# Optimization experiments

Measured on AMD Instinct MI355X. Metric: run time of the kernel, lower is better.

## Reference

```python
import jax, jax.numpy as jnp
import numpy as np

DIM = 1024
NUM_HEADS = 16
HEAD_DIM = DIM // NUM_HEADS


def setup_inputs() -> dict:
    key = jax.random.key(0)
    ks = jax.random.split(key, 5)
    scale = 1.0 / np.sqrt(DIM)
    return {
        "x": jax.random.normal(ks[0], (2, 2048, DIM), dtype=jnp.float32),
        "qkv_w": jax.random.normal(ks[1], (3 * DIM, DIM), dtype=jnp.float32) * scale,
        "qkv_b": jax.random.normal(ks[2], (3 * DIM,), dtype=jnp.float32) * 0.01,
        "proj_w": jax.random.normal(ks[3], (DIM, DIM), dtype=jnp.float32) * scale,
        "proj_b": jax.random.normal(ks[4], (DIM,), dtype=jnp.float32) * 0.01,
    }


def reference(x, qkv_w, qkv_b, proj_w, proj_b):
    B, N, D = x.shape
    H, Hd = NUM_HEADS, HEAD_DIM
    # fused QKV projection: [B,N,3D]
    qkv = jnp.einsum('bnd,ed->bne', x, qkv_w) + qkv_b
    qkv = qkv.reshape(B, N, 3, H, Hd)
    q = qkv[:, :, 0].transpose(0, 2, 1, 3)  # [B,H,N,Hd]
    k = qkv[:, :, 1].transpose(0, 2, 1, 3)
    v = qkv[:, :, 2].transpose(0, 2, 1, 3)
    scale = 1.0 / jnp.sqrt(jnp.asarray(Hd, dtype=x.dtype))
    scores = jnp.einsum('bhqd,bhkd->bhqk', q, k) * scale  # [B,H,N,N]
    attn = jax.nn.softmax(scores, axis=-1)
    out = jnp.einsum('bhqk,bhkd->bhqd', attn, v)  # [B,H,N,Hd]
    out = out.transpose(0, 2, 1, 3).reshape(B, N, D)
    return jnp.einsum('bnd,ed->bne', out, proj_w) + proj_b
```

## Files before the change

kernel.cpp:

```cpp
#include <hip/hip_runtime.h>
#include <hip/hip_bf16.h>
#include <stdint.h>


typedef __bf16 bf16;
typedef __bf16 bf16x2 __attribute__((ext_vector_type(2)));
typedef __bf16 bf16x4 __attribute__((ext_vector_type(4)));
typedef __bf16 bf16x8 __attribute__((ext_vector_type(8)));
typedef float  f32x4  __attribute__((ext_vector_type(4)));
typedef float  f32x16 __attribute__((ext_vector_type(16)));
typedef uint32_t u32x4 __attribute__((ext_vector_type(4)));

#define QSCALE 0.18033688011112042f

__device__ __forceinline__ void gload_lds16(const void* g, void* l) {
    __builtin_amdgcn_global_load_lds(
        (const __attribute__((address_space(1))) void*)(uintptr_t)g,
        (__attribute__((address_space(3))) void*)(uint32_t)(uintptr_t)l,
        16, 0, 0);
}

__device__ __forceinline__ uint32_t pkbf(float a, float b) {
    bf16x2 t = { (bf16)a, (bf16)b };
    return __builtin_bit_cast(uint32_t, t);
}

__global__ void cast_all(const float* __restrict__ x,
                         const float* __restrict__ qw,
                         const float* __restrict__ pw,
                         bf16* __restrict__ xb, bf16* __restrict__ wq,
                         bf16* __restrict__ wp) {
    int i = blockIdx.x * blockDim.x + threadIdx.x;
    const float4* src; bf16x4* dst; int off;
    if (i < 1048576)      { src = (const float4*)x;  dst = (bf16x4*)xb; off = i; }
    else if (i < 1835008) { src = (const float4*)qw; dst = (bf16x4*)wq; off = i - 1048576; }
    else                  { src = (const float4*)pw; dst = (bf16x4*)wp; off = i - 1835008; }
    float4 v = src[off];
    bf16x4 o = { (bf16)v.x, (bf16)v.y, (bf16)v.z, (bf16)v.w };
    dst[off] = o;
}

template<int EPI>
__global__ __launch_bounds__(256) void gemm128(
    const bf16* __restrict__ A,
    const bf16* __restrict__ Bw,
    const float* __restrict__ bias,
    float* __restrict__ outF,
    bf16* __restrict__ qb, bf16* __restrict__ kf, bf16* __restrict__ vf,
    int K)
{
    __shared__ __align__(16) char gsm[EPI == 0 ? 36864 : 32768];
    bf16* ct = (bf16*)gsm;
    const int tid  = threadIdx.x;
    const int lane = tid & 63, w = tid >> 6;
    const int g = lane >> 4, lr = lane & 15;
    const int wr = w >> 1, wc = w & 1;
    int mt, nt;
    if (EPI == 0) {
        int bid = blockIdx.x;
        int xcd = bid & 7, i = bid >> 3;
        mt = xcd * 4 + i / 24;
        nt = i % 24;
    } else {
        nt = blockIdx.x; mt = blockIdx.y;
    }
    const int mbase = mt * 128, nbase = nt * 128;

    f32x4 acc[4][4] = {};

    auto stg = [&](int buf, int it) {
        const bf16* Ag = A  + (size_t)mbase * K + it * 32;
        const bf16* Bg = Bw + (size_t)nbase * K + it * 32;
        bf16* as = (bf16*)(gsm + buf * 16384);
        bf16* bs = (bf16*)(gsm + buf * 16384 + 8192);
        int c0 = tid, c1 = 256 + tid;
        gload_lds16(Ag + (size_t)(c0 >> 2) * K + (c0 & 3) * 8, as + c0 * 8);
        gload_lds16(Bg + (size_t)(c0 >> 2) * K + (c0 & 3) * 8, bs + c0 * 8);
        gload_lds16(Ag + (size_t)(c1 >> 2) * K + (c1 & 3) * 8, as + c1 * 8);
        gload_lds16(Bg + (size_t)(c1 >> 2) * K + (c1 & 3) * 8, bs + c1 * 8);
    };

    const int nIt = K >> 5;
    stg(0, 0);
    __syncthreads();

    #pragma unroll 2
    for (int it = 0; it < nIt; ++it) {
        const int cur = it & 1;
        if (it + 1 < nIt) stg(cur ^ 1, it + 1);

        const bf16* as = (const bf16*)(gsm + cur * 16384);
        const bf16* bs = as + 4096;
        bf16x8 af[4], bfr[4];
        #pragma unroll
        for (int mi = 0; mi < 4; ++mi)
            af[mi] = *(const bf16x8*)(as + (wr * 64 + mi * 16 + lr) * 32 + g * 8);
        #pragma unroll
        for (int ni = 0; ni < 4; ++ni)
            bfr[ni] = *(const bf16x8*)(bs + (wc * 64 + ni * 16 + lr) * 32 + g * 8);
        #pragma unroll
        for (int mi = 0; mi < 4; ++mi)
            #pragma unroll
            for (int ni = 0; ni < 4; ++ni)
                acc[mi][ni] = __builtin_amdgcn_mfma_f32_16x16x32_bf16(
                    af[mi], bfr[ni], acc[mi][ni], 0, 0, 0);

        __syncthreads();
    }

    if (EPI == 1) {
        #pragma unroll
        for (int ni = 0; ni < 4; ++ni) {
            int e = nbase + wc * 64 + ni * 16 + lr;
            float bv = bias[e];
            #pragma unroll
            for (int mi = 0; mi < 4; ++mi) {
                #pragma unroll
                for (int r = 0; r < 4; ++r) {
                    int token = mbase + wr * 64 + mi * 16 + g * 4 + r;
                    outF[(size_t)token * 1024 + e] = acc[mi][ni][r] + bv;
                }
            }
        }
    } else {
        const int sec = nbase >> 10;
        #pragma unroll
        for (int ni = 0; ni < 4; ++ni) {
            int ec = wc * 64 + ni * 16 + lr;
            float bv = bias[nbase + ec];
            #pragma unroll
            for (int mi = 0; mi < 4; ++mi) {
                #pragma unroll
                for (int r = 0; r < 4; ++r) {
                    int tl = wr * 64 + mi * 16 + g * 4 + r;
                    float v = acc[mi][ni][r] + bv;
                    if (sec == 0) v *= QSCALE;
                    int row = (sec == 2) ? ec : tl;
                    int col = (sec == 2) ? tl : ec;
                    ct[row * 144 + col] = (bf16)v;
                }
            }
        }
        __syncthreads();
        const int b  = mbase >> 11;
        const int h0 = (nbase & 1023) >> 6;
        const int mb = mbase & 2047;
        #pragma unroll
        for (int si = 0; si < 8; ++si) {
            int c   = si * 256 + tid;
            int hh  = c >> 10;
            int w10 = c & 1023;
            int bh  = b * 16 + h0 + hh;
            int lrow, lcol;
            size_t gaddr;
            bf16* dst;
            if (sec == 0) {
                int nl = w10 >> 3, d0 = (w10 & 7) * 8;
                lrow = nl; lcol = hh * 64 + d0;
                gaddr = ((size_t)bh * 2048 + mb + nl) * 64 + d0;
                dst = qb;
            } else if (sec == 1) {
                int o = w10 * 8;
                int frag = o >> 9, l = (o >> 3) & 63;
                int nl = (frag >> 2) * 32 + (l & 31);
                int d0 = (frag & 3) * 16 + (l >> 5) * 8;
                lrow = nl; lcol = hh * 64 + d0;
                gaddr = ((size_t)(bh * 64 + (mb >> 5))) * 2048 + o;
                dst = kf;
            } else {
                int o = w10 * 8;
                int n6 = o >> 12, r2 = o & 4095;
                int d5 = r2 >> 11, r3 = r2 & 2047;
                int nc = r3 >> 9,  l  = (r3 >> 3) & 63;
                int d  = d5 * 32 + (l & 31);
                int n0 = n6 * 64 + nc * 16 + (l >> 5) * 8;
                lrow = hh * 64 + d; lcol = n0;
                gaddr = ((size_t)(bh * 32 + (mb >> 6))) * 4096 + o;
                dst = vf;
            }
            *(bf16x8*)(dst + gaddr) = *(const bf16x8*)(&ct[lrow * 144 + lcol]);
        }
    }
}

__global__ __launch_bounds__(512, 4) void attn32(
    const bf16* __restrict__ Q,
    const bf16* __restrict__ Kf,
    const bf16* __restrict__ Vf,
    bf16* __restrict__ Ao,
    int Nseq)
{
    __shared__ __align__(16) char smem[65536];
    bf16*  KsB = (bf16*)smem;
    bf16*  VsB = (bf16*)(smem + 32768);
    float* xch = (float*)smem;
    bf16*  otp = (bf16*)(smem + 36864);

    const int tid  = threadIdx.x;
    const int lane = tid & 63;
    const int u    = tid >> 6;
    const int half = u >> 2, qw = u & 3;
    const int hi = lane >> 5, ql = lane & 31;
    const int bid = blockIdx.x;
    const int xcd = bid & 7, ii = bid >> 3;
    const int bh = xcd * 4 + (ii >> 4), qc = ii & 15;
    const int h = bh & 15, b = bh >> 4;
    const int q0 = qc * 128 + qw * 32;

    const bf16* Qh  = Q  + (size_t)bh * Nseq * 64;
    const bf16* Kfh = Kf + (size_t)bh * Nseq * 64;
    const bf16* Vfh = Vf + (size_t)bh * Nseq * 64;

    bf16x8 qf[4];
    #pragma unroll
    for (int c = 0; c < 4; ++c)
        qf[c] = *(const bf16x8*)(Qh + (size_t)(q0 + ql) * 64 + c * 16 + hi * 8);

    bf16x8 vones;
    #pragma unroll
    for (int i = 0; i < 8; ++i) vones[i] = (bf16)1.0f;

    f32x16 o0 = {}, o1 = {};
    f32x16 la = {};

    const int nch = (Nseq >> 6) >> 1;
    const int hk  = half * nch;

    auto stage = [&](int buf, int t) {
        const bf16* Kc = Kfh + (size_t)(hk + t) * 4096;
        const bf16* Vc = Vfh + (size_t)(hk + t) * 4096;
        bf16* kd = KsB + (half * 2 + buf) * 4096;
        bf16* vd = VsB + (half * 2 + buf) * 4096;
        int ht = tid & 255;
        gload_lds16(Kc + ht * 8,        kd + ht * 8);
        gload_lds16(Kc + 2048 + ht * 8, kd + 2048 + ht * 8);
        gload_lds16(Vc + ht * 8,        vd + ht * 8);
        gload_lds16(Vc + 2048 + ht * 8, vd + 2048 + ht * 8);
    };

    stage(0, 0);
    __syncthreads();

    #pragma unroll 2
    for (int t = 0; t < nch; ++t) {
        const int cur = t & 1;
        if (t + 1 < nch) stage(cur ^ 1, t + 1);

        const bf16* kl = KsB + (half * 2 + cur) * 4096;
        const bf16* vl = VsB + (half * 2 + cur) * 4096;
        bf16x8 kin[8], vfr[8];
        #pragma unroll
        for (int i = 0; i < 8; ++i)
            kin[i] = *(const bf16x8*)(kl + i * 512 + lane * 8);
        #pragma unroll
        for (int i = 0; i < 8; ++i)
            vfr[i] = *(const bf16x8*)(vl + i * 512 + lane * 8);

        f32x16 s0 = {}, s1 = {};
        #pragma unroll
        for (int c = 0; c < 4; ++c) {
            s0 = __builtin_amdgcn_mfma_f32_32x32x16_bf16(kin[c],     qf[c], s0, 0, 0, 0);
            s1 = __builtin_amdgcn_mfma_f32_32x32x16_bf16(kin[4 + c], qf[c], s1, 0, 0, 0);
        }

        float p0[16], p1[16];
        #pragma unroll
        for (int r = 0; r < 16; ++r) { p0[r] = __builtin_amdgcn_exp2f(s0[r]); }
        #pragma unroll
        for (int r = 0; r < 16; ++r) { p1[r] = __builtin_amdgcn_exp2f(s1[r]); }

        bf16x8 pfr[4];
        #pragma unroll
        for (int f = 0; f < 4; ++f) {
            const float* pp = (f < 2) ? p0 : p1;
            const int base = (f & 1) * 8;
            union { uint32_t u[4]; bf16x8 v; } pw;
            #pragma unroll
            for (int wd = 0; wd < 2; ++wd) {
                uint32_t X = pkbf(pp[base + 2*wd], pp[base + 2*wd + 1]);
                uint32_t Y = pkbf(pp[base + 4 + 2*wd], pp[base + 4 + 2*wd + 1]);
                auto rr = __builtin_amdgcn_permlane32_swap((int)X, (int)Y, false, false);
                pw.u[wd]     = (uint32_t)rr[0];
                pw.u[2 + wd] = (uint32_t)rr[1];
            }
            pfr[f] = pw.v;
        }

        #pragma unroll
        for (int f = 0; f < 4; ++f) {
            o0 = __builtin_amdgcn_mfma_f32_32x32x16_bf16(vfr[f],     pfr[f], o0, 0, 0, 0);
            o1 = __builtin_amdgcn_mfma_f32_32x32x16_bf16(vfr[4 + f], pfr[f], o1, 0, 0, 0);
            la = __builtin_amdgcn_mfma_f32_32x32x16_bf16(vones,      pfr[f], la, 0, 0, 0);
        }

        __syncthreads();
    }

    float lsum = la[0];

    if (half == 1) {
        float* xp = xch + ((size_t)(qw * 64 + lane)) * 36;
        *(f32x16*)(xp)      = o0;
        *(f32x16*)(xp + 16) = o1;
        xp[32] = lsum;
    }
    __syncthreads();
    if (half == 0) {
        const float* xp = xch + ((size_t)(qw * 64 + lane)) * 36;
        f32x16 oa = *(const f32x16*)(xp);
        f32x16 ob = *(const f32x16*)(xp + 16);
        o0 += oa; o1 += ob; lsum += xp[32];

        float linv = __builtin_amdgcn_rcpf(lsum);

        #pragma unroll
        for (int qd = 0; qd < 4; ++qd) {
            int dbase = 8 * qd + 4 * hi;
            bf16* orow = otp + (qw * 32 + ql) * 66;
            *(uint32_t*)(orow + dbase)          = pkbf(o0[4*qd] * linv,   o0[4*qd+1] * linv);
            *(uint32_t*)(orow + dbase + 2)      = pkbf(o0[4*qd+2] * linv, o0[4*qd+3] * linv);
            *(uint32_t*)(orow + 32 + dbase)     = pkbf(o1[4*qd] * linv,   o1[4*qd+1] * linv);
            *(uint32_t*)(orow + 32 + dbase + 2) = pkbf(o1[4*qd+2] * linv, o1[4*qd+3] * linv);
        }
        __asm__ volatile("s_waitcnt lgkmcnt(0)" ::: "memory");
        const int t = lane >> 1, e = lane & 1;
        uint32_t rw[16];
        #pragma unroll
        for (int j = 0; j < 16; ++j)
            rw[j] = *(const uint32_t*)(otp + (qw * 32 + t) * 66 + e * 32 + 2 * j);
        size_t gbase = (size_t)(b * Nseq + q0 + t) * 1024 + h * 64 + e * 32;
        #pragma unroll
        for (int v = 0; v < 4; ++v) {
            u32x4 sv = { rw[4*v], rw[4*v+1], rw[4*v+2], rw[4*v+3] };
            *(u32x4*)(Ao + gbase + v * 8) = sv;
        }
    }
}

extern "C" void kernel_launch(void* const* d_in, const int* in_sizes, int n_in,
                              void* d_out, int out_size, void* d_ws, size_t ws_size,
                              hipStream_t stream) {
    const float* x      = (const float*)d_in[0];
    const float* qkv_w  = (const float*)d_in[1];
    const float* qkv_b  = (const float*)d_in[2];
    const float* proj_w = (const float*)d_in[3];
    const float* proj_b = (const float*)d_in[4];
    float* out = (float*)d_out;

    char* ws = (char*)d_ws;
    bf16* xb    = (bf16*)(ws);
    bf16* wqkv  = (bf16*)(ws + ((size_t)8  << 20));
    bf16* wproj = (bf16*)(ws + ((size_t)14 << 20));
    bf16* qb    = (bf16*)(ws + ((size_t)16 << 20));
    bf16* kf    = (bf16*)(ws + ((size_t)24 << 20));
    bf16* vf    = (bf16*)(ws + ((size_t)32 << 20));
    bf16* att   = (bf16*)(ws);

    cast_all<<<dim3(8192), dim3(256), 0, stream>>>(x, qkv_w, proj_w, xb, wqkv, wproj);

    gemm128<0><<<dim3(768), dim3(256), 0, stream>>>(
        xb, wqkv, qkv_b, (float*)nullptr, qb, kf, vf, 1024);

    attn32<<<dim3(512), dim3(512), 0, stream>>>(qb, kf, vf, att, 2048);

    gemm128<1><<<dim3(8, 32), dim3(256), 0, stream>>>(
        att, wproj, proj_b, out, (bf16*)nullptr, (bf16*)nullptr, (bf16*)nullptr, 1024);
}
```

Before: 111.1 us.

## Process two 32-row query tiles per wave in attention to reuse K/V fragments

Each wave of the attention kernel now handles 64 query rows, as two 32-row tiles, instead of 32. The K and V fragments it loads from LDS are reused for both tiles, and the grid is halved to 256 blocks. This halves the LDS reads and global K/V staging per query row. In exchange, register use roughly doubles, launch bounds drop to 2 blocks per CU, and 256 blocks may underfill the 256 CUs with fewer waves to hide latency.

```diff
diff --git a/kernel.cpp b/kernel.cpp
--- a/kernel.cpp
+++ b/kernel.cpp
@@ -183,7 +183,7 @@
     }
 }
 
-__global__ __launch_bounds__(512, 4) void attn32(
+__global__ __launch_bounds__(512, 2) void attn32(
     const bf16* __restrict__ Q,
     const bf16* __restrict__ Kf,
     const bf16* __restrict__ Vf,
@@ -203,25 +203,27 @@
     const int hi = lane >> 5, ql = lane & 31;
     const int bid = blockIdx.x;
     const int xcd = bid & 7, ii = bid >> 3;
-    const int bh = xcd * 4 + (ii >> 4), qc = ii & 15;
+    const int bh = xcd * 4 + (ii >> 3), qc = ii & 7;
     const int h = bh & 15, b = bh >> 4;
-    const int q0 = qc * 128 + qw * 32;
+    const int q0 = qc * 256 + qw * 64;
 
     const bf16* Qh  = Q  + (size_t)bh * Nseq * 64;
     const bf16* Kfh = Kf + (size_t)bh * Nseq * 64;
     const bf16* Vfh = Vf + (size_t)bh * Nseq * 64;
 
-    bf16x8 qf[4];
+    bf16x8 qfA[4], qfB[4];
     #pragma unroll
-    for (int c = 0; c < 4; ++c)
-        qf[c] = *(const bf16x8*)(Qh + (size_t)(q0 + ql) * 64 + c * 16 + hi * 8);
+    for (int c = 0; c < 4; ++c) {
+        qfA[c] = *(const bf16x8*)(Qh + (size_t)(q0 + ql) * 64 + c * 16 + hi * 8);
+        qfB[c] = *(const bf16x8*)(Qh + (size_t)(q0 + 32 + ql) * 64 + c * 16 + hi * 8);
+    }
 
     bf16x8 vones;
     #pragma unroll
     for (int i = 0; i < 8; ++i) vones[i] = (bf16)1.0f;
 
-    f32x16 o0 = {}, o1 = {};
-    f32x16 la = {};
+    f32x16 o0A = {}, o1A = {}, laA = {};
+    f32x16 o0B = {}, o1B = {}, laB = {};
 
     const int nch = (Nseq >> 6) >> 1;
     const int hk  = half * nch;
@@ -256,85 +258,123 @@
         for (int i = 0; i < 8; ++i)
             vfr[i] = *(const bf16x8*)(vl + i * 512 + lane * 8);
 
-        f32x16 s0 = {}, s1 = {};
-        #pragma unroll
-        for (int c = 0; c < 4; ++c) {
-            s0 = __builtin_amdgcn_mfma_f32_32x32x16_bf16(kin[c],     qf[c], s0, 0, 0, 0);
-            s1 = __builtin_amdgcn_mfma_f32_32x32x16_bf16(kin[4 + c], qf[c], s1, 0, 0, 0);
-        }
-
-        float p0[16], p1[16];
-        #pragma unroll
-        for (int r = 0; r < 16; ++r) { p0[r] = __builtin_amdgcn_exp2f(s0[r]); }
-        #pragma unroll
-        for (int r = 0; r < 16; ++r) { p1[r] = __builtin_amdgcn_exp2f(s1[r]); }
-
-        bf16x8 pfr[4];
-        #pragma unroll
-        for (int f = 0; f < 4; ++f) {
-            const float* pp = (f < 2) ? p0 : p1;
-            const int base = (f & 1) * 8;
-            union { uint32_t u[4]; bf16x8 v; } pw;
-            #pragma unroll
-            for (int wd = 0; wd < 2; ++wd) {
-                uint32_t X = pkbf(pp[base + 2*wd], pp[base + 2*wd + 1]);
-                uint32_t Y = pkbf(pp[base + 4 + 2*wd], pp[base + 4 + 2*wd + 1]);
-                auto rr = __builtin_amdgcn_permlane32_swap((int)X, (int)Y, false, false);
-                pw.u[wd]     = (uint32_t)rr[0];
-                pw.u[2 + wd] = (uint32_t)rr[1];
-            }
-            pfr[f] = pw.v;
-        }
-
-        #pragma unroll
-        for (int f = 0; f < 4; ++f) {
-            o0 = __builtin_amdgcn_mfma_f32_32x32x16_bf16(vfr[f],     pfr[f], o0, 0, 0, 0);
-            o1 = __builtin_amdgcn_mfma_f32_32x32x16_bf16(vfr[4 + f], pfr[f], o1, 0, 0, 0);
-            la = __builtin_amdgcn_mfma_f32_32x32x16_bf16(vones,      pfr[f], la, 0, 0, 0);
+        {
+            f32x16 s0 = {}, s1 = {};
+            #pragma unroll
+            for (int c = 0; c < 4; ++c) {
+                s0 = __builtin_amdgcn_mfma_f32_32x32x16_bf16(kin[c],     qfA[c], s0, 0, 0, 0);
+                s1 = __builtin_amdgcn_mfma_f32_32x32x16_bf16(kin[4 + c], qfA[c], s1, 0, 0, 0);
+            }
+            float p0[16], p1[16];
+            #pragma unroll
+            for (int r = 0; r < 16; ++r) { p0[r] = __builtin_amdgcn_exp2f(s0[r]); }
+            #pragma unroll
+            for (int r = 0; r < 16; ++r) { p1[r] = __builtin_amdgcn_exp2f(s1[r]); }
+            bf16x8 pfr[4];
+            #pragma unroll
+            for (int f = 0; f < 4; ++f) {
+                const float* pp = (f < 2) ? p0 : p1;
+                const int base = (f & 1) * 8;
+                union { uint32_t u[4]; bf16x8 v; } pw;
+                #pragma unroll
+                for (int wd = 0; wd < 2; ++wd) {
+                    uint32_t X = pkbf(pp[base + 2*wd], pp[base + 2*wd + 1]);
+                    uint32_t Y = pkbf(pp[base + 4 + 2*wd], pp[base + 4 + 2*wd + 1]);
+                    auto rr = __builtin_amdgcn_permlane32_swap((int)X, (int)Y, false, false);
+                    pw.u[wd]     = (uint32_t)rr[0];
+                    pw.u[2 + wd] = (uint32_t)rr[1];
+                }
+                pfr[f] = pw.v;
+            }
+            #pragma unroll
+            for (int f = 0; f < 4; ++f) {
+                o0A = __builtin_amdgcn_mfma_f32_32x32x16_bf16(vfr[f],     pfr[f], o0A, 0, 0, 0);
+                o1A = __builtin_amdgcn_mfma_f32_32x32x16_bf16(vfr[4 + f], pfr[f], o1A, 0, 0, 0);
+                laA = __builtin_amdgcn_mfma_f32_32x32x16_bf16(vones,      pfr[f], laA, 0, 0, 0);
+            }
+        }
+        {
+            f32x16 s0 = {}, s1 = {};
+            #pragma unroll
+            for (int c = 0; c < 4; ++c) {
+                s0 = __builtin_amdgcn_mfma_f32_32x32x16_bf16(kin[c],     qfB[c], s0, 0, 0, 0);
+                s1 = __builtin_amdgcn_mfma_f32_32x32x16_bf16(kin[4 + c], qfB[c], s1, 0, 0, 0);
+            }
+            float p0[16], p1[16];
+            #pragma unroll
+            for (int r = 0; r < 16; ++r) { p0[r] = __builtin_amdgcn_exp2f(s0[r]); }
+            #pragma unroll
+            for (int r = 0; r < 16; ++r) { p1[r] = __builtin_amdgcn_exp2f(s1[r]); }
+            bf16x8 pfr[4];
+            #pragma unroll
+            for (int f = 0; f < 4; ++f) {
+                const float* pp = (f < 2) ? p0 : p1;
+                const int base = (f & 1) * 8;
+                union { uint32_t u[4]; bf16x8 v; } pw;
+                #pragma unroll
+                for (int wd = 0; wd < 2; ++wd) {
+                    uint32_t X = pkbf(pp[base + 2*wd], pp[base + 2*wd + 1]);
+                    uint32_t Y = pkbf(pp[base + 4 + 2*wd], pp[base + 4 + 2*wd + 1]);
+                    auto rr = __builtin_amdgcn_permlane32_swap((int)X, (int)Y, false, false);
+                    pw.u[wd]     = (uint32_t)rr[0];
+                    pw.u[2 + wd] = (uint32_t)rr[1];
+                }
+                pfr[f] = pw.v;
+            }
+            #pragma unroll
+            for (int f = 0; f < 4; ++f) {
+                o0B = __builtin_amdgcn_mfma_f32_32x32x16_bf16(vfr[f],     pfr[f], o0B, 0, 0, 0);
+                o1B = __builtin_amdgcn_mfma_f32_32x32x16_bf16(vfr[4 + f], pfr[f], o1B, 0, 0, 0);
+                laB = __builtin_amdgcn_mfma_f32_32x32x16_bf16(vones,      pfr[f], laB, 0, 0, 0);
+            }
         }
 
         __syncthreads();
     }
 
-    float lsum = la[0];
-
-    if (half == 1) {
-        float* xp = xch + ((size_t)(qw * 64 + lane)) * 36;
-        *(f32x16*)(xp)      = o0;
-        *(f32x16*)(xp + 16) = o1;
-        xp[32] = lsum;
-    }
-    __syncthreads();
-    if (half == 0) {
-        const float* xp = xch + ((size_t)(qw * 64 + lane)) * 36;
-        f32x16 oa = *(const f32x16*)(xp);
-        f32x16 ob = *(const f32x16*)(xp + 16);
-        o0 += oa; o1 += ob; lsum += xp[32];
-
-        float linv = __builtin_amdgcn_rcpf(lsum);
-
-        #pragma unroll
-        for (int qd = 0; qd < 4; ++qd) {
-            int dbase = 8 * qd + 4 * hi;
-            bf16* orow = otp + (qw * 32 + ql) * 66;
-            *(uint32_t*)(orow + dbase)          = pkbf(o0[4*qd] * linv,   o0[4*qd+1] * linv);
-            *(uint32_t*)(orow + dbase + 2)      = pkbf(o0[4*qd+2] * linv, o0[4*qd+3] * linv);
-            *(uint32_t*)(orow + 32 + dbase)     = pkbf(o1[4*qd] * linv,   o1[4*qd+1] * linv);
-            *(uint32_t*)(orow + 32 + dbase + 2) = pkbf(o1[4*qd+2] * linv, o1[4*qd+3] * linv);
-        }
-        __asm__ volatile("s_waitcnt lgkmcnt(0)" ::: "memory");
-        const int t = lane >> 1, e = lane & 1;
-        uint32_t rw[16];
-        #pragma unroll
-        for (int j = 0; j < 16; ++j)
-            rw[j] = *(const uint32_t*)(otp + (qw * 32 + t) * 66 + e * 32 + 2 * j);
-        size_t gbase = (size_t)(b * Nseq + q0 + t) * 1024 + h * 64 + e * 32;
-        #pragma unroll
-        for (int v = 0; v < 4; ++v) {
-            u32x4 sv = { rw[4*v], rw[4*v+1], rw[4*v+2], rw[4*v+3] };
-            *(u32x4*)(Ao + gbase + v * 8) = sv;
-        }
-    }
+    auto finish = [&](const f32x16& po0, const f32x16& po1, const f32x16& pla, int qp) {
+        float lsum = pla[0];
+        __syncthreads();
+        if (half == 1) {
+            float* xp = xch + ((size_t)(qw * 64 + lane)) * 36;
+            *(f32x16*)(xp)      = po0;
+            *(f32x16*)(xp + 16) = po1;
+            xp[32] = lsum;
+        }
+        __syncthreads();
+        if (half == 0) {
+            const float* xp = xch + ((size_t)(qw * 64 + lane)) * 36;
+            f32x16 oa = *(const f32x16*)(xp);
+            f32x16 ob = *(const f32x16*)(xp + 16);
+            f32x16 m0 = po0 + oa;
+            f32x16 m1 = po1 + ob;
+            float ls = lsum + xp[32];
+            float linv = __builtin_amdgcn_rcpf(ls);
+            #pragma unroll
+            for (int qd = 0; qd < 4; ++qd) {
+                int dbase = 8 * qd + 4 * hi;
+                bf16* orow = otp + (qw * 32 + ql) * 66;
+                *(uint32_t*)(orow + dbase)          = pkbf(m0[4*qd] * linv,   m0[4*qd+1] * linv);
+                *(uint32_t*)(orow + dbase + 2)      = pkbf(m0[4*qd+2] * linv, m0[4*qd+3] * linv);
+                *(uint32_t*)(orow + 32 + dbase)     = pkbf(m1[4*qd] * linv,   m1[4*qd+1] * linv);
+                *(uint32_t*)(orow + 32 + dbase + 2) = pkbf(m1[4*qd+2] * linv, m1[4*qd+3] * linv);
+            }
+            __asm__ volatile("s_waitcnt lgkmcnt(0)" ::: "memory");
+            const int t = lane >> 1, e = lane & 1;
+            uint32_t rw[16];
+            #pragma unroll
+            for (int j = 0; j < 16; ++j)
+                rw[j] = *(const uint32_t*)(otp + (qw * 32 + t) * 66 + e * 32 + 2 * j);
+            size_t gbase = (size_t)(b * Nseq + q0 + qp + t) * 1024 + h * 64 + e * 32;
+            #pragma unroll
+            for (int v = 0; v < 4; ++v) {
+                u32x4 sv = { rw[4*v], rw[4*v+1], rw[4*v+2], rw[4*v+3] };
+                *(u32x4*)(Ao + gbase + v * 8) = sv;
+            }
+        }
+    };
+    finish(o0A, o1A, laA, 0);
+    finish(o0B, o1B, laB, 32);
 }
 
 extern "C" void kernel_launch(void* const* d_in, const int* in_sizes, int n_in,
@@ -361,7 +401,7 @@
     gemm128<0><<<dim3(768), dim3(256), 0, stream>>>(
         xb, wqkv, qkv_b, (float*)nullptr, qb, kf, vf, 1024);
 
-    attn32<<<dim3(512), dim3(512), 0, stream>>>(qb, kf, vf, att, 2048);
+    attn32<<<dim3(256), dim3(512), 0, stream>>>(qb, kf, vf, att, 2048);
 
     gemm128<1><<<dim3(8, 32), dim3(256), 0, stream>>>(
         att, wproj, proj_b, out, (bf16*)nullptr, (bf16*)nullptr, (bf16*)nullptr, 1024);
```

Result: faster. 106.8 us (median of 2 runs) (-3.9%).
